# Kernel optimization log

Measured on AMD Instinct MI355X. Metric: run time of the kernel, lower is better.

The kernel has to match this reference:

```python
import jax, jax.numpy as jnp
import numpy as np

N_QUBITS = 14
STATE_DIM = 2 ** N_QUBITS  # 16384
BATCH, SEQ = 4, 2048


def setup_inputs() -> dict:
    key = jax.random.key(0)
    ks = jax.random.split(key, 5)
    x = jax.random.normal(ks[0], (BATCH, SEQ), dtype=jnp.float32)
    rotation_params = jax.random.normal(ks[1], (N_QUBITS, 3), dtype=jnp.float32)
    entangling_params = jax.random.normal(ks[2], (N_QUBITS - 1,), dtype=jnp.float32)
    # classical_encoder: Linear(1, n_qubits) -> Tanh -> Linear(n_qubits, state_dim) -> Softmax
    W1 = jax.random.normal(ks[3], (1, N_QUBITS), dtype=jnp.float32)
    b1 = jnp.zeros((N_QUBITS,), dtype=jnp.float32)
    W2 = jax.random.normal(ks[4], (N_QUBITS, STATE_DIM), dtype=jnp.float32) * 0.1
    b2 = jnp.zeros((STATE_DIM,), dtype=jnp.float32)
    return {"x": x, "rotation_params": rotation_params,
            "entangling_params": entangling_params,
            "W1": W1, "b1": b1, "W2": W2, "b2": b2}


def reference(x, rotation_params, entangling_params, W1, b1, W2, b2):
    # classical_encoder applied to each scalar x[i,j] -> softmax weights [B,S,D]
    h = jnp.tanh(x[..., None] * W1[0] + b1)          # [B,S,nq]
    w = jax.nn.softmax(h @ W2 + b2, axis=-1)         # [B,S,D]
    # Per-qubit rotation scalar factors (independent of x), multiplied together
    half = rotation_params * 0.5
    c, s = jnp.cos(half), jnp.sin(half)              # [nq,3]
    rot_factors = c[:, 0] * c[:, 1] * c[:, 2] + 1j * (s[:, 0] * s[:, 1] * s[:, 2])
    # Per-pair parameterized-CNOT scalar factors
    cs = jax.nn.sigmoid(entangling_params)
    ent_factors = cs + 1j * (1.0 - cs)
    total = (jnp.prod(rot_factors) * jnp.prod(ent_factors)).astype(jnp.complex64)
    # state starts as e0; all scalar multiplies keep only component 0 nonzero,
    # then elementwise multiply by classical weights.
    out = jnp.zeros(w.shape, dtype=jnp.complex64)
    out = out.at[..., 0].set(total * w[..., 0].astype(jnp.complex64))
    return out
```

## Files before the change

kernel.cpp:

```cpp
#include <hip/hip_runtime.h>
#include <math.h>

constexpr int NQ    = 14;
constexpr int DIM   = 16384;
constexpr int BATCH = 4;
constexpr int SEQ   = 2048;
constexpr int NPOS  = BATCH * SEQ;
constexpr int TPB   = 256;
constexpr int P     = 16;
constexpr int NBLK  = NPOS / P;


template <bool CPLX>
__global__ void __launch_bounds__(TPB)
qenc_compute(const float* __restrict__ x,
             const float* __restrict__ rot,
             const float* __restrict__ ent,
             const float* __restrict__ W1,
             const float* __restrict__ b1,
             const float* __restrict__ W2,
             const float* __restrict__ b2,
             float* __restrict__ out)
{
    __shared__ float sh_h[P * 16];
    __shared__ float red[4][P];
    __shared__ float sh_tot_re, sh_tot_im;

    const int tid  = threadIdx.x;
    const int wid  = tid >> 6;
    const int lane = tid & 63;
    const long long pos0 = (long long)blockIdx.x * P;

    if (tid < P * NQ) {
        const int p = tid / NQ;
        const int k = tid - p * NQ;
        sh_h[p * 16 + k] = tanhf(x[pos0 + p] * W1[k] + b1[k]);
    }
    if (tid == 240) {
        float tre = 1.0f, tim = 0.0f;
        for (int q = 0; q < NQ; ++q) {
            const float a0 = 0.5f * rot[q * 3 + 0];
            const float a1 = 0.5f * rot[q * 3 + 1];
            const float a2 = 0.5f * rot[q * 3 + 2];
            const float fre = cosf(a0) * cosf(a1) * cosf(a2);
            const float fim = sinf(a0) * sinf(a1) * sinf(a2);
            const float nre = tre * fre - tim * fim;
            const float nim = tre * fim + tim * fre;
            tre = nre; tim = nim;
        }
        for (int q = 0; q < NQ - 1; ++q) {
            const float cs  = 1.0f / (1.0f + __expf(-ent[q]));
            const float nre = tre * cs - tim * (1.0f - cs);
            const float nim = tre * (1.0f - cs) + tim * cs;
            tre = nre; tim = nim;
        }
        sh_tot_re = tre; sh_tot_im = tim;
    }
    __syncthreads();

    float acc[P];
#pragma unroll
    for (int p = 0; p < P; ++p) acc[p] = 0.0f;

    constexpr int ITERS = DIM / (4 * TPB);
    for (int i = 0; i < ITERS; ++i) {
        const int d = 4 * (tid + TPB * i);
        float4 wv[NQ];
#pragma unroll
        for (int k = 0; k < NQ; ++k)
            wv[k] = *reinterpret_cast<const float4*>(W2 + (size_t)k * DIM + d);
        const float4 bb = *reinterpret_cast<const float4*>(b2 + d);

#pragma unroll
        for (int p = 0; p < P; ++p) {
            const float4 ha = *reinterpret_cast<const float4*>(&sh_h[p * 16 + 0]);
            const float4 hb = *reinterpret_cast<const float4*>(&sh_h[p * 16 + 4]);
            const float4 hc = *reinterpret_cast<const float4*>(&sh_h[p * 16 + 8]);
            const float2 he = *reinterpret_cast<const float2*>(&sh_h[p * 16 + 12]);
            const float hh[NQ] = {ha.x, ha.y, ha.z, ha.w,
                                  hb.x, hb.y, hb.z, hb.w,
                                  hc.x, hc.y, hc.z, hc.w,
                                  he.x, he.y};
            float za = bb.x, zb = bb.y, zc = bb.z, zd = bb.w;
#pragma unroll
            for (int k = 0; k < NQ; ++k) {
                za = fmaf(hh[k], wv[k].x, za);
                zb = fmaf(hh[k], wv[k].y, zb);
                zc = fmaf(hh[k], wv[k].z, zc);
                zd = fmaf(hh[k], wv[k].w, zd);
            }
            acc[p] += (__expf(za) + __expf(zb)) + (__expf(zc) + __expf(zd));
        }
    }

#pragma unroll
    for (int p = 0; p < P; ++p) {
        float v = acc[p];
#pragma unroll
        for (int off = 32; off > 0; off >>= 1)
            v += __shfl_down(v, off, 64);
        if (lane == 0) red[wid][p] = v;
    }
    __syncthreads();

    if (tid < P) {
        const float denom = (red[0][tid] + red[1][tid]) + (red[2][tid] + red[3][tid]);
        float z0 = b2[0];
#pragma unroll
        for (int k = 0; k < NQ; ++k)
            z0 = fmaf(sh_h[tid * 16 + k], W2[(size_t)k * DIM], z0);
        const float w0 = __expf(z0) / denom;
        const size_t stride = CPLX ? 2 * (size_t)DIM : (size_t)DIM;
        float* rowp = out + (size_t)(pos0 + tid) * stride;
        rowp[0] = sh_tot_re * w0;
        if constexpr (CPLX) rowp[1] = sh_tot_im * w0;
    }
}

extern "C" void kernel_launch(void* const* d_in, const int* in_sizes, int n_in,
                              void* d_out, int out_size, void* d_ws, size_t ws_size,
                              hipStream_t stream) {
    (void)in_sizes; (void)n_in; (void)d_ws; (void)ws_size;
    const float* x   = (const float*)d_in[0];
    const float* rot = (const float*)d_in[1];
    const float* ent = (const float*)d_in[2];
    const float* W1  = (const float*)d_in[3];
    const float* b1  = (const float*)d_in[4];
    const float* W2  = (const float*)d_in[5];
    const float* b2  = (const float*)d_in[6];
    float* out = (float*)d_out;

    const long long cplx_elems = (long long)NPOS * 2LL * DIM;
    if ((long long)out_size >= cplx_elems) {
        hipMemsetAsync(d_out, 0, (size_t)NPOS * 2 * (size_t)DIM * sizeof(float), stream);
        qenc_compute<true><<<NBLK, TPB, 0, stream>>>(x, rot, ent, W1, b1, W2, b2, out);
    } else {
        hipMemsetAsync(d_out, 0, (size_t)NPOS * (size_t)DIM * sizeof(float), stream);
        qenc_compute<false><<<NBLK, TPB, 0, stream>>>(x, rot, ent, W1, b1, W2, b2, out);
    }
}
```

Measured before the change: 635.0 us.

## Fuse output zero-fill into compute kernel and split positions per wavefront

Replaces the separate hipMemsetAsync with extra blocks in a single launch that write zeros to each output row except its first four floats, using nontemporal stores. Compute blocks now give each wavefront its own 4 positions over the full dimension, which removes the cross-wave shared-memory reduction and second barrier. The h values are read into wave-uniform registers, and each row's first float4 is written as one vector store. This removes a separate memset pass and a sync. In exchange, each wave loads all of W2 on its own, and zero-fill blocks share the GPU with compute blocks.

```diff
diff --git a/kernel.cpp b/kernel.cpp
--- a/kernel.cpp
+++ b/kernel.cpp
@@ -7,34 +7,61 @@
 constexpr int SEQ   = 2048;
 constexpr int NPOS  = BATCH * SEQ;
 constexpr int TPB   = 256;
-constexpr int P     = 16;
-constexpr int NBLK  = NPOS / P;
+
+constexpr int PCOMP = 16;
+constexpr int NCOMP = NPOS / PCOMP;
+constexpr int RPF   = 2;
+constexpr int NFILL = NPOS / RPF;
+
+typedef float vf4 __attribute__((ext_vector_type(4)));
+
+__device__ __forceinline__ float uniform_f(float v) {
+    return __int_as_float(__builtin_amdgcn_readfirstlane(__float_as_int(v)));
+}
 
 
 template <bool CPLX>
 __global__ void __launch_bounds__(TPB)
-qenc_compute(const float* __restrict__ x,
-             const float* __restrict__ rot,
-             const float* __restrict__ ent,
-             const float* __restrict__ W1,
-             const float* __restrict__ b1,
-             const float* __restrict__ W2,
-             const float* __restrict__ b2,
-             float* __restrict__ out)
+qenc_mega(const float* __restrict__ x,
+          const float* __restrict__ rot,
+          const float* __restrict__ ent,
+          const float* __restrict__ W1,
+          const float* __restrict__ b1,
+          const float* __restrict__ W2,
+          const float* __restrict__ b2,
+          float* __restrict__ out)
 {
-    __shared__ float sh_h[P * 16];
-    __shared__ float red[4][P];
+    constexpr size_t ROW_F = CPLX ? 2 * (size_t)DIM : (size_t)DIM;
+    const int tid = threadIdx.x;
+
+    if (blockIdx.x >= NCOMP) {
+        const size_t fb = (size_t)blockIdx.x - NCOMP;
+        float* row = out + fb * RPF * ROW_F;
+        constexpr int Q4 = (int)(ROW_F / 4) - 1;
+        constexpr int J  = (Q4 + TPB - 1) / TPB;
+        vf4 z = {0.f, 0.f, 0.f, 0.f};
+#pragma unroll
+        for (int j = 0; j < J; ++j) {
+            const int i = tid + TPB * j;
+            if (i < Q4) {
+                __builtin_nontemporal_store(z, reinterpret_cast<vf4*>(row + 4 + 4 * (size_t)i));
+                __builtin_nontemporal_store(z, reinterpret_cast<vf4*>(row + ROW_F + 4 + 4 * (size_t)i));
+            }
+        }
+        return;
+    }
+
+    __shared__ float sh_h[PCOMP][NQ];
     __shared__ float sh_tot_re, sh_tot_im;
 
-    const int tid  = threadIdx.x;
     const int wid  = tid >> 6;
     const int lane = tid & 63;
-    const long long pos0 = (long long)blockIdx.x * P;
+    const long long pos0 = (long long)blockIdx.x * PCOMP;
 
-    if (tid < P * NQ) {
+    if (tid < PCOMP * NQ) {
         const int p = tid / NQ;
         const int k = tid - p * NQ;
-        sh_h[p * 16 + k] = tanhf(x[pos0 + p] * W1[k] + b1[k]);
+        sh_h[p][k] = tanhf(x[pos0 + p] * W1[k] + b1[k]);
     }
     if (tid == 240) {
         float tre = 1.0f, tim = 0.0f;
@@ -58,62 +85,56 @@
     }
     __syncthreads();
 
-    float acc[P];
+    float h[4][NQ];
 #pragma unroll
-    for (int p = 0; p < P; ++p) acc[p] = 0.0f;
+    for (int q = 0; q < 4; ++q)
+#pragma unroll
+        for (int k = 0; k < NQ; ++k)
+            h[q][k] = uniform_f(sh_h[wid * 4 + q][k]);
 
-    constexpr int ITERS = DIM / (4 * TPB);
-    for (int i = 0; i < ITERS; ++i) {
-        const int d = 4 * (tid + TPB * i);
+    float acc[4] = {0.f, 0.f, 0.f, 0.f};
+    float z0[4]  = {0.f, 0.f, 0.f, 0.f};
+
+    constexpr int ITERS = DIM / (4 * 64);
+    for (int ii = 0; ii < ITERS; ++ii) {
+        const int d = 4 * (lane + 64 * ii);
         float4 wv[NQ];
 #pragma unroll
         for (int k = 0; k < NQ; ++k)
             wv[k] = *reinterpret_cast<const float4*>(W2 + (size_t)k * DIM + d);
         const float4 bb = *reinterpret_cast<const float4*>(b2 + d);
-
 #pragma unroll
-        for (int p = 0; p < P; ++p) {
-            const float4 ha = *reinterpret_cast<const float4*>(&sh_h[p * 16 + 0]);
-            const float4 hb = *reinterpret_cast<const float4*>(&sh_h[p * 16 + 4]);
-            const float4 hc = *reinterpret_cast<const float4*>(&sh_h[p * 16 + 8]);
-            const float2 he = *reinterpret_cast<const float2*>(&sh_h[p * 16 + 12]);
-            const float hh[NQ] = {ha.x, ha.y, ha.z, ha.w,
-                                  hb.x, hb.y, hb.z, hb.w,
-                                  hc.x, hc.y, hc.z, hc.w,
-                                  he.x, he.y};
+        for (int q = 0; q < 4; ++q) {
             float za = bb.x, zb = bb.y, zc = bb.z, zd = bb.w;
 #pragma unroll
             for (int k = 0; k < NQ; ++k) {
-                za = fmaf(hh[k], wv[k].x, za);
-                zb = fmaf(hh[k], wv[k].y, zb);
-                zc = fmaf(hh[k], wv[k].z, zc);
-                zd = fmaf(hh[k], wv[k].w, zd);
+                za = fmaf(h[q][k], wv[k].x, za);
+                zb = fmaf(h[q][k], wv[k].y, zb);
+                zc = fmaf(h[q][k], wv[k].z, zc);
+                zd = fmaf(h[q][k], wv[k].w, zd);
             }
-            acc[p] += (__expf(za) + __expf(zb)) + (__expf(zc) + __expf(zd));
+            if (d == 0) z0[q] = za;
+            acc[q] += (__expf(za) + __expf(zb)) + (__expf(zc) + __expf(zd));
         }
     }
 
 #pragma unroll
-    for (int p = 0; p < P; ++p) {
-        float v = acc[p];
+    for (int q = 0; q < 4; ++q) {
 #pragma unroll
         for (int off = 32; off > 0; off >>= 1)
-            v += __shfl_down(v, off, 64);
-        if (lane == 0) red[wid][p] = v;
+            acc[q] += __shfl_down(acc[q], off, 64);
     }
-    __syncthreads();
 
-    if (tid < P) {
-        const float denom = (red[0][tid] + red[1][tid]) + (red[2][tid] + red[3][tid]);
-        float z0 = b2[0];
+    if (lane == 0) {
+        const float tre = sh_tot_re, tim = sh_tot_im;
 #pragma unroll
-        for (int k = 0; k < NQ; ++k)
-            z0 = fmaf(sh_h[tid * 16 + k], W2[(size_t)k * DIM], z0);
-        const float w0 = __expf(z0) / denom;
-        const size_t stride = CPLX ? 2 * (size_t)DIM : (size_t)DIM;
-        float* rowp = out + (size_t)(pos0 + tid) * stride;
-        rowp[0] = sh_tot_re * w0;
-        if constexpr (CPLX) rowp[1] = sh_tot_im * w0;
+        for (int q = 0; q < 4; ++q) {
+            const float w0 = __expf(z0[q]) / acc[q];
+            vf4 v;
+            if constexpr (CPLX) v = {tre * w0, tim * w0, 0.f, 0.f};
+            else                v = {tre * w0, 0.f, 0.f, 0.f};
+            *reinterpret_cast<vf4*>(out + (size_t)(pos0 + wid * 4 + q) * ROW_F) = v;
+        }
     }
 }
 
@@ -132,10 +153,8 @@
 
     const long long cplx_elems = (long long)NPOS * 2LL * DIM;
     if ((long long)out_size >= cplx_elems) {
-        hipMemsetAsync(d_out, 0, (size_t)NPOS * 2 * (size_t)DIM * sizeof(float), stream);
-        qenc_compute<true><<<NBLK, TPB, 0, stream>>>(x, rot, ent, W1, b1, W2, b2, out);
+        qenc_mega<true><<<NCOMP + NFILL, TPB, 0, stream>>>(x, rot, ent, W1, b1, W2, b2, out);
     } else {
-        hipMemsetAsync(d_out, 0, (size_t)NPOS * (size_t)DIM * sizeof(float), stream);
-        qenc_compute<false><<<NBLK, TPB, 0, stream>>>(x, rot, ent, W1, b1, W2, b2, out);
+        qenc_mega<false><<<NCOMP + NFILL, TPB, 0, stream>>>(x, rot, ent, W1, b1, W2, b2, out);
     }
 }
```

New measurement: 633.3 us. No clear change (-0.3%).

## Fuse output zero-fill into compute kernel via dedicated fill blocks

Applied to the files above, without the earlier changes.

Removes the separate hipMemsetAsync and has the kernel launch extra blocks that zero every 16-byte chunk of the output except each row's head. The compute blocks write the head as a full vec4 holding the result and zeros. This lets the compute-bound softmax work and the bandwidth-bound zero fill of about 1 GB of complex output run at the same time inside one launch, and saves one launch. The risk is that the fill blocks compete with the compute blocks for CUs and that a hand-written fill may reach lower bandwidth than the driver memset.

```diff
diff --git a/kernel.cpp b/kernel.cpp
--- a/kernel.cpp
+++ b/kernel.cpp
@@ -7,31 +7,51 @@
 constexpr int SEQ   = 2048;
 constexpr int NPOS  = BATCH * SEQ;
 constexpr int TPB   = 256;
-constexpr int P     = 16;
-constexpr int NBLK  = NPOS / P;
+
+constexpr int PCOMP = 16;
+constexpr int NCOMP = NPOS / PCOMP;
+constexpr int NFILL = 1024;
+
+typedef float vf4 __attribute__((ext_vector_type(4)));
 
 
 template <bool CPLX>
 __global__ void __launch_bounds__(TPB)
-qenc_compute(const float* __restrict__ x,
-             const float* __restrict__ rot,
-             const float* __restrict__ ent,
-             const float* __restrict__ W1,
-             const float* __restrict__ b1,
-             const float* __restrict__ W2,
-             const float* __restrict__ b2,
-             float* __restrict__ out)
+qenc_split(const float* __restrict__ x,
+           const float* __restrict__ rot,
+           const float* __restrict__ ent,
+           const float* __restrict__ W1,
+           const float* __restrict__ b1,
+           const float* __restrict__ W2,
+           const float* __restrict__ b2,
+           float* __restrict__ out)
 {
-    __shared__ float sh_h[P * 16];
-    __shared__ float red[4][P];
+    constexpr size_t ROW_F  = CPLX ? 2 * (size_t)DIM : (size_t)DIM;
+    constexpr size_t HEADS4 = ROW_F / 4;
+    constexpr size_t TOT4   = (size_t)NPOS * HEADS4;
+    const int tid = threadIdx.x;
+
+    if (blockIdx.x >= NCOMP) {
+        const size_t gtid    = ((size_t)blockIdx.x - NCOMP) * TPB + tid;
+        const size_t gstride = (size_t)NFILL * TPB;
+        vf4 z = {0.f, 0.f, 0.f, 0.f};
+#pragma unroll 8
+        for (size_t i4 = gtid; i4 < TOT4; i4 += gstride) {
+            if ((i4 & (HEADS4 - 1)) != 0)
+                *reinterpret_cast<vf4*>(out + 4 * i4) = z;
+        }
+        return;
+    }
+
+    __shared__ float sh_h[PCOMP * 16];
+    __shared__ float red[4][PCOMP];
     __shared__ float sh_tot_re, sh_tot_im;
 
-    const int tid  = threadIdx.x;
     const int wid  = tid >> 6;
     const int lane = tid & 63;
-    const long long pos0 = (long long)blockIdx.x * P;
+    const long long pos0 = (long long)blockIdx.x * PCOMP;
 
-    if (tid < P * NQ) {
+    if (tid < PCOMP * NQ) {
         const int p = tid / NQ;
         const int k = tid - p * NQ;
         sh_h[p * 16 + k] = tanhf(x[pos0 + p] * W1[k] + b1[k]);
@@ -58,9 +78,9 @@
     }
     __syncthreads();
 
-    float acc[P];
+    float acc[PCOMP];
 #pragma unroll
-    for (int p = 0; p < P; ++p) acc[p] = 0.0f;
+    for (int p = 0; p < PCOMP; ++p) acc[p] = 0.0f;
 
     constexpr int ITERS = DIM / (4 * TPB);
     for (int i = 0; i < ITERS; ++i) {
@@ -72,7 +92,7 @@
         const float4 bb = *reinterpret_cast<const float4*>(b2 + d);
 
 #pragma unroll
-        for (int p = 0; p < P; ++p) {
+        for (int p = 0; p < PCOMP; ++p) {
             const float4 ha = *reinterpret_cast<const float4*>(&sh_h[p * 16 + 0]);
             const float4 hb = *reinterpret_cast<const float4*>(&sh_h[p * 16 + 4]);
             const float4 hc = *reinterpret_cast<const float4*>(&sh_h[p * 16 + 8]);
@@ -94,7 +114,7 @@
     }
 
 #pragma unroll
-    for (int p = 0; p < P; ++p) {
+    for (int p = 0; p < PCOMP; ++p) {
         float v = acc[p];
 #pragma unroll
         for (int off = 32; off > 0; off >>= 1)
@@ -103,17 +123,17 @@
     }
     __syncthreads();
 
-    if (tid < P) {
+    if (tid < PCOMP) {
         const float denom = (red[0][tid] + red[1][tid]) + (red[2][tid] + red[3][tid]);
         float z0 = b2[0];
 #pragma unroll
         for (int k = 0; k < NQ; ++k)
             z0 = fmaf(sh_h[tid * 16 + k], W2[(size_t)k * DIM], z0);
         const float w0 = __expf(z0) / denom;
-        const size_t stride = CPLX ? 2 * (size_t)DIM : (size_t)DIM;
-        float* rowp = out + (size_t)(pos0 + tid) * stride;
-        rowp[0] = sh_tot_re * w0;
-        if constexpr (CPLX) rowp[1] = sh_tot_im * w0;
+        vf4 head;
+        if constexpr (CPLX) head = {sh_tot_re * w0, sh_tot_im * w0, 0.f, 0.f};
+        else                head = {sh_tot_re * w0, 0.f, 0.f, 0.f};
+        *reinterpret_cast<vf4*>(out + (size_t)(pos0 + tid) * ROW_F) = head;
     }
 }
 
@@ -132,10 +152,8 @@
 
     const long long cplx_elems = (long long)NPOS * 2LL * DIM;
     if ((long long)out_size >= cplx_elems) {
-        hipMemsetAsync(d_out, 0, (size_t)NPOS * 2 * (size_t)DIM * sizeof(float), stream);
-        qenc_compute<true><<<NBLK, TPB, 0, stream>>>(x, rot, ent, W1, b1, W2, b2, out);
+        qenc_split<true><<<NCOMP + NFILL, TPB, 0, stream>>>(x, rot, ent, W1, b1, W2, b2, out);
     } else {
-        hipMemsetAsync(d_out, 0, (size_t)NPOS * (size_t)DIM * sizeof(float), stream);
-        qenc_compute<false><<<NBLK, TPB, 0, stream>>>(x, rot, ent, W1, b1, W2, b2, out);
+        qenc_split<false><<<NCOMP + NFILL, TPB, 0, stream>>>(x, rot, ent, W1, b1, W2, b2, out);
     }
 }
```

New measurement: 675.3 us. 1.06x slower.
